# Kernel optimization log

Measured on AMD Instinct MI355X. Metric: run time of the kernel, lower is better.

The kernel has to match this reference:

```python
import jax, jax.numpy as jnp
import numpy as np

B, S, HID = 1, 2048, 2048
HQ, HKV, D = 16, 4, 128
BS = 64            # seerattn gate block size
GH = 128           # gate hidden size
INTER = 5632
THR = 0.004        # seerattn_threshold on softmaxed block gate scores
EPS = 1e-6
NEG = -1e30


def _rms(x, w):
    xf = x.astype(jnp.float32)
    var = jnp.mean(xf * xf, axis=-1, keepdims=True)
    return (w * (xf * jax.lax.rsqrt(var + EPS))).astype(x.dtype)


def _rotate_half(x):
    x1, x2 = jnp.split(x, 2, axis=-1)
    return jnp.concatenate([-x2, x1], axis=-1)


def setup_inputs() -> dict:
    key = jax.random.key(0)
    ks = jax.random.split(key, 16)
    s = 0.02
    pos = jnp.arange(S, dtype=jnp.float32)
    inv_freq = 1.0 / (1e6 ** (jnp.arange(0, D, 2, dtype=jnp.float32) / D))
    freqs = pos[:, None] * inv_freq[None, :]
    emb = jnp.concatenate([freqs, freqs], axis=-1)  # [S, D]
    return {
        'hidden_states': jax.random.normal(ks[0], (B, S, HID), jnp.float32),
        'cos': jnp.cos(emb),
        'sin': jnp.sin(emb),
        'ln1_w': jnp.ones((HID,), jnp.float32),
        'ln2_w': jnp.ones((HID,), jnp.float32),
        'Wq': jax.random.normal(ks[1], (HID, HQ * D), jnp.float32) * s,
        'bq': jnp.zeros((HQ * D,), jnp.float32),
        'Wk': jax.random.normal(ks[2], (HID, HKV * D), jnp.float32) * s,
        'bk': jnp.zeros((HKV * D,), jnp.float32),
        'Wv': jax.random.normal(ks[3], (HID, HKV * D), jnp.float32) * s,
        'bv': jnp.zeros((HKV * D,), jnp.float32),
        'Wo': jax.random.normal(ks[4], (HQ * D, HID), jnp.float32) * s,
        'gWq': jax.random.normal(ks[5], (D, GH), jnp.float32) * s,
        'gWk': jax.random.normal(ks[6], (D, GH), jnp.float32) * s,
        'Wgate': jax.random.normal(ks[7], (HID, INTER), jnp.float32) * s,
        'Wup': jax.random.normal(ks[8], (HID, INTER), jnp.float32) * s,
        'Wdown': jax.random.normal(ks[9], (INTER, HID), jnp.float32) * s,
    }


def reference(hidden_states, cos, sin, ln1_w, ln2_w, Wq, bq, Wk, bk, Wv, bv, Wo,
              gWq, gWk, Wgate, Wup, Wdown):
    B_, S_, _ = hidden_states.shape
    QB = S_ // BS
    grp = HQ // HKV

    h = _rms(hidden_states, ln1_w)
    q = (h @ Wq + bq).reshape(B_, S_, HQ, D)
    k = (h @ Wk + bk).reshape(B_, S_, HKV, D)
    v = (h @ Wv + bv).reshape(B_, S_, HKV, D)

    # ---- learned block gate (pre-RoPE q/k), threshold sparsity method ----
    qg = jnp.einsum('bshd,dg->bshg', q, gWq)
    qg = qg.reshape(B_, QB, BS, HQ, GH).mean(axis=2)            # [B, QB, HQ, GH]
    kp = k.reshape(B_, QB, BS, HKV, D).mean(axis=2)             # block-pooled K
    kg = jnp.einsum('bkhd,dg->bkhg', kp, gWk)
    kg = jnp.repeat(kg, grp, axis=2)                            # GQA -> HQ heads
    gscore = jnp.einsum('bqhg,bkhg->bhqk', qg, kg) * (GH ** -0.5)

    bidx = jnp.arange(QB)
    blk_causal = bidx[:, None] >= bidx[None, :]                 # [QB, QB]
    gscore = jnp.where(blk_causal[None, None], gscore, NEG)
    gate = jax.nn.softmax(gscore, axis=-1)                      # [B, HQ, QB, QB]

    diag = bidx[:, None] == bidx[None, :]
    keep = blk_causal[None, None] & ((gate >= THR) | diag[None, None])

    # ---- RoPE (unsqueeze_dim=2, layout [B,S,H,D]) ----
    c = cos[None, :, None, :]
    sn = sin[None, :, None, :]
    q = q * c + _rotate_half(q) * sn
    k = k * c + _rotate_half(k) * sn

    k = jnp.repeat(k, grp, axis=2)
    v = jnp.repeat(v, grp, axis=2)

    # ---- block-sparse masked attention (reference: dense w/ block mask) ----
    scores = jnp.einsum('bqhd,bkhd->bhqk', q, k) * (D ** -0.5)
    tok_keep = jnp.repeat(jnp.repeat(keep, BS, axis=2), BS, axis=3)
    tidx = jnp.arange(S_)
    tok_causal = tidx[:, None] >= tidx[None, :]
    mask = tok_keep & tok_causal[None, None]
    scores = jnp.where(mask, scores, NEG)
    p = jax.nn.softmax(scores, axis=-1)
    o = jnp.einsum('bhqk,bkhd->bqhd', p, v).reshape(B_, S_, HQ * D)
    attn_out = o @ Wo

    h2 = hidden_states + attn_out
    h3 = _rms(h2, ln2_w)
    mlp = (jax.nn.silu(h3 @ Wgate) * (h3 @ Wup)) @ Wdown
    return h2 + mlp
```

## Files before the change

kernel.cpp:

```cpp
#include <hip/hip_runtime.h>
#include <stdint.h>
#include <stddef.h>

#define S_LEN 2048
#define HIDN  2048
#define HQ    16
#define HKV   4
#define HDIM  128
#define NQKV  3072
#define QBLK  32
#define GHW   128
#define INTER 5632
#define NEGF  (-1e30f)
#define THRG  0.004f

typedef short bf16x8 __attribute__((ext_vector_type(8)));
typedef float f32x4  __attribute__((ext_vector_type(4)));

__device__ __forceinline__ short f2bf(float f) {
  union { float f; unsigned u; } v; v.f = f;
  unsigned r = (v.u + 0x7FFFu + ((v.u >> 16) & 1u)) >> 16;
  return (short)r;
}
__device__ __forceinline__ float bf2f(short s) {
  union { float f; unsigned u; } v; v.u = ((unsigned)(unsigned short)s) << 16;
  return v.f;
}
__device__ __forceinline__ void gload16(const void* g, void* l) {
  __builtin_amdgcn_global_load_lds(
      (const __attribute__((address_space(1))) void*)g,
      (__attribute__((address_space(3))) void*)l, 16, 0, 0);
}
__device__ __forceinline__ unsigned pack_bf2(float hi, float lo) {
  return __builtin_amdgcn_perm(__float_as_uint(hi), __float_as_uint(lo), 0x07060302u);
}

__global__ __launch_bounds__(256) void k_transpose_cast(
    const float* __restrict__ src, short* __restrict__ dst, int R, int C) {
  __shared__ float t[32][33];
  const int tx = threadIdx.x, ty = threadIdx.y;
  const int x = blockIdx.x * 32 + tx;
  const int y0 = blockIdx.y * 32;
#pragma unroll
  for (int i = 0; i < 4; i++) {
    int yy = ty + i * 8;
    t[yy][tx] = src[(long)(y0 + yy) * C + x];
  }
  __syncthreads();
  const int xo = blockIdx.y * 32 + tx;
  const int yo0 = blockIdx.x * 32;
#pragma unroll
  for (int i = 0; i < 4; i++) {
    int yy = ty + i * 8;
    dst[(long)(yo0 + yy) * R + xo] = f2bf(t[tx][yy]);
  }
}

__global__ __launch_bounds__(256) void k_transpose_cast_ilv(
    const float* __restrict__ src, short* __restrict__ dst, int R, int C, int phase) {
  __shared__ float t[32][33];
  const int tx = threadIdx.x, ty = threadIdx.y;
  const int x = blockIdx.x * 32 + tx;
  const int y0 = blockIdx.y * 32;
#pragma unroll
  for (int i = 0; i < 4; i++) {
    int yy = ty + i * 8;
    t[yy][tx] = src[(long)(y0 + yy) * C + x];
  }
  __syncthreads();
  const int xo = blockIdx.y * 32 + tx;
  const int yo0 = blockIdx.x * 32;
#pragma unroll
  for (int i = 0; i < 4; i++) {
    int j = yo0 + ty + i * 8;
    long orow = (long)(j >> 4) * 32 + phase * 16 + (j & 15);
    dst[orow * R + xo] = f2bf(t[tx][ty + i * 8]);
  }
}

__global__ void k_bias_concat(const float* __restrict__ bq, const float* __restrict__ bk,
                              const float* __restrict__ bv, float* __restrict__ out) {
  int i = blockIdx.x * 256 + threadIdx.x;
  if (i < 2048) out[i] = bq[i];
  else if (i < 2560) out[i] = bk[i - 2048];
  else out[i] = bv[i - 2560];
}

__global__ __launch_bounds__(256) void k_rms(const float* __restrict__ x,
                                             const float* __restrict__ w,
                                             short* __restrict__ out) {
  const int row = blockIdx.x;
  const float* xr = x + (long)row * HIDN;
  float v[8];
  float ss = 0.f;
#pragma unroll
  for (int i = 0; i < 8; i++) {
    v[i] = xr[threadIdx.x + i * 256];
    ss += v[i] * v[i];
  }
#pragma unroll
  for (int off = 32; off > 0; off >>= 1) ss += __shfl_down(ss, off, 64);
  __shared__ float red[4];
  const int wave = threadIdx.x >> 6, lane = threadIdx.x & 63;
  if (lane == 0) red[wave] = ss;
  __syncthreads();
  float tot = red[0] + red[1] + red[2] + red[3];
  float rs = rsqrtf(tot / (float)HIDN + 1e-6f);
#pragma unroll
  for (int i = 0; i < 8; i++) {
    int c = threadIdx.x + i * 256;
    out[(long)row * HIDN + c] = f2bf(v[i] * rs * w[c]);
  }
}

__global__ __launch_bounds__(256) void k_rms_fin(const float* __restrict__ p0,
                                                 const float* __restrict__ hid,
                                                 const float* __restrict__ w,
                                                 float* __restrict__ h2,
                                                 short* __restrict__ out) {
  const int row = blockIdx.x;
  const long base = (long)row * HIDN;
  float v[8];
  float ss = 0.f;
#pragma unroll
  for (int i = 0; i < 8; i++) {
    int c = threadIdx.x + i * 256;
    float t = p0[base + c] + h2[base + c] + hid[base + c];
    h2[base + c] = t;
    v[i] = t;
    ss += t * t;
  }
#pragma unroll
  for (int off = 32; off > 0; off >>= 1) ss += __shfl_down(ss, off, 64);
  __shared__ float red[4];
  const int wave = threadIdx.x >> 6, lane = threadIdx.x & 63;
  if (lane == 0) red[wave] = ss;
  __syncthreads();
  float tot = red[0] + red[1] + red[2] + red[3];
  float rs = rsqrtf(tot / (float)HIDN + 1e-6f);
#pragma unroll
  for (int i = 0; i < 8; i++) {
    int c = threadIdx.x + i * 256;
    out[base + c] = f2bf(v[i] * rs * w[c]);
  }
}

template <int MODE, int BN>
__global__ __launch_bounds__(256) void k_gemm(
    const short* __restrict__ A, const short* __restrict__ Bt,
    float* __restrict__ Cf, float* __restrict__ Cf2,
    short* __restrict__ Cb,
    const float* __restrict__ bias, const float* __restrict__ add,
    int M, int N, int K, int ksl) {
  constexpr int NT = BN / 32;
  constexpr int BIW = BN / 32;
  constexpr int BPP = BN / 16;
  __shared__ short As[2][128][32];
  __shared__ short Bs[2][BN][32];
  const int tid = threadIdx.x;
  const int wave = tid >> 6, lane = tid & 63, quad = lane >> 4, l15 = lane & 15;
  const long m0 = (long)blockIdx.y * 128, n0 = (long)blockIdx.x * BN;
  const int wr = (wave >> 1) * 64, wc = (wave & 1) * (BN / 2);
  const int i2 = lane >> 2, i3 = lane & 3;
  f32x4 acc[4][NT] = {};
  const short* Ainst[4];
  short* Alds[4];
#pragma unroll
  for (int j = 0; j < 4; j++) {
    const int g = wave * 4 + j, h = g >> 3, rb = (g & 7) * 16;
    Ainst[j] = A + (m0 + rb + i2) * K + h * 32 + i3 * 8;
    Alds[j] = &As[h][rb][0];
  }
  const short* Binst[BIW];
  short* Blds[BIW];
#pragma unroll
  for (int j = 0; j < BIW; j++) {
    const int g = wave * BIW + j, h = g / BPP, rb = (g % BPP) * 16;
    Binst[j] = Bt + (n0 + rb + i2) * K + h * 32 + i3 * 8;
    Blds[j] = &Bs[h][rb][0];
  }
  const int kbeg = (MODE == 4) ? blockIdx.z * ksl : 0;
  const int kend = kbeg + ((MODE == 4) ? ksl : K);
  for (int k0 = kbeg; k0 < kend; k0 += 64) {
    __syncthreads();
#pragma unroll
    for (int j = 0; j < 4; j++) gload16(Ainst[j] + k0, Alds[j]);
#pragma unroll
    for (int j = 0; j < BIW; j++) gload16(Binst[j] + k0, Blds[j]);
    __syncthreads();
#pragma unroll
    for (int s = 0; s < 2; s++) {
      bf16x8 af[4], bb[NT];
#pragma unroll
      for (int mi = 0; mi < 4; mi++)
        af[mi] = *(const bf16x8*)&As[s][wr + mi * 16 + l15][quad * 8];
#pragma unroll
      for (int ni = 0; ni < NT; ni++)
        bb[ni] = *(const bf16x8*)&Bs[s][wc + ni * 16 + l15][quad * 8];
#pragma unroll
      for (int mi = 0; mi < 4; mi++)
#pragma unroll
        for (int ni = 0; ni < NT; ni++)
          acc[mi][ni] = __builtin_amdgcn_mfma_f32_16x16x32_bf16(af[mi], bb[ni], acc[mi][ni], 0, 0, 0);
    }
  }
  const bool hb = (MODE == 0) && (bias != nullptr);
  const bool ha = (MODE == 0) && (add != nullptr);
  float* dstp = (MODE == 4) ? ((blockIdx.z == 0) ? Cf : Cf2) : Cf;
#pragma unroll
  for (int mi = 0; mi < 4; mi++) {
    if (MODE == 5) {
#pragma unroll
      for (int ni2 = 0; ni2 < NT / 2; ni2++) {
        long mbase = m0 + wr + mi * 16 + quad * 4;
        long col = (n0 + wc) / 2 + ni2 * 16 + l15;
#pragma unroll
        for (int r = 0; r < 4; r++) {
          float g = acc[mi][2 * ni2][r];
          float u = acc[mi][2 * ni2 + 1][r];
          float sg = g / (1.f + __expf(-g));
          Cb[(mbase + r) * INTER + col] = f2bf(sg * u);
        }
      }
    } else {
#pragma unroll
      for (int ni = 0; ni < NT; ni++) {
        long mbase = m0 + wr + mi * 16 + quad * 4;
        long n = n0 + wc + ni * 16 + l15;
#pragma unroll
        for (int r = 0; r < 4; r++) {
          float v = acc[mi][ni][r];
          if (MODE == 0) {
            long idx = (mbase + r) * N + n;
            if (hb) v += bias[n];
            if (ha) v += add[idx];
            Cf[idx] = v;
          } else {
            dstp[(mbase + r) * N + n] = v;
          }
        }
      }
    }
  }
}

__global__ __launch_bounds__(256) void k_finish(const float* __restrict__ p0,
                                                const float* __restrict__ h2,
                                                float* __restrict__ out) {
  const long n = (long)S_LEN * HIDN;
  for (long i = ((long)blockIdx.x * 256 + threadIdx.x) * 4; i < n;
       i += (long)gridDim.x * 256 * 4) {
    float4 a = *(const float4*)(out + i);
    float4 b = *(const float4*)(p0 + i);
    float4 c = *(const float4*)(h2 + i);
    a.x += b.x + c.x;
    a.y += b.y + c.y;
    a.z += b.z + c.z;
    a.w += b.w + c.w;
    *(float4*)(out + i) = a;
  }
}

__global__ __launch_bounds__(256) void k_blockmean(const float* __restrict__ qkv,
                                                   float* __restrict__ qm,
                                                   float* __restrict__ km) {
  int id = blockIdx.x * 256 + threadIdx.x;
  int qb = id / 2560, c = id % 2560;
  const float* base = qkv + (long)qb * 64 * NQKV + c;
  float acc = 0.f;
  for (int s = 0; s < 64; s++) acc += base[(long)s * NQKV];
  acc *= (1.f / 64.f);
  if (c < 2048) qm[(long)qb * 2048 + c] = acc;
  else km[(long)qb * 512 + (c - 2048)] = acc;
}

__global__ __launch_bounds__(128) void k_gateproj(const float* __restrict__ qm,
                                                  const float* __restrict__ km,
                                                  const float* __restrict__ gWq,
                                                  const float* __restrict__ gWk,
                                                  float* __restrict__ qg,
                                                  float* __restrict__ kg) {
  __shared__ float xm[128];
  const int b = blockIdx.x;
  const float* src; const float* W; float* dst;
  if (b < 512) { src = qm + (long)b * 128; W = gWq; dst = qg + (long)b * 128; }
  else { int r = b - 512; src = km + (long)r * 128; W = gWk; dst = kg + (long)r * 128; }
  xm[threadIdx.x] = src[threadIdx.x];
  __syncthreads();
  float acc = 0.f;
  for (int d = 0; d < 128; d++) acc += xm[d] * W[d * GHW + threadIdx.x];
  dst[threadIdx.x] = acc;
}

__global__ __launch_bounds__(64) void k_gatemask(const float* __restrict__ qg,
                                                 const float* __restrict__ kg,
                                                 unsigned char* __restrict__ mask) {
  const int qb = blockIdx.x, h = blockIdx.y;
  __shared__ float qv[128];
  const int t = threadIdx.x;
  qv[t] = qg[((long)qb * 16 + h) * 128 + t];
  qv[t + 64] = qg[((long)qb * 16 + h) * 128 + t + 64];
  __syncthreads();
  const int kb = t;
  float s = NEGF;
  if (kb < 32 && kb <= qb) {
    const float* kr = kg + ((long)kb * 4 + (h >> 2)) * 128;
    float acc = 0.f;
    for (int d = 0; d < 128; d++) acc += qv[d] * kr[d];
    s = acc * 0.08838834764831845f;
  }
  float m = s;
#pragma unroll
  for (int off = 32; off > 0; off >>= 1) m = fmaxf(m, __shfl_xor(m, off, 64));
  float e = (kb < 32 && kb <= qb) ? __expf(s - m) : 0.f;
  float sum = e;
#pragma unroll
  for (int off = 32; off > 0; off >>= 1) sum += __shfl_xor(sum, off, 64);
  if (kb < 32) {
    float gate = e / sum;
    bool keep = (kb <= qb) && (gate >= THRG || kb == qb);
    mask[((long)h * 32 + qb) * 32 + kb] = keep ? 1 : 0;
  }
}

__global__ __launch_bounds__(256) void k_rope(const float* __restrict__ qkv,
                                              const float* __restrict__ cosb,
                                              const float* __restrict__ sinb,
                                              short* __restrict__ q_bf,
                                              short* __restrict__ k_bf) {
  long id = (long)blockIdx.x * 256 + threadIdx.x;
  int d = (int)(id & 63);
  long rest = id >> 6;
  int head = (int)(rest % 20);
  int s = (int)(rest / 20);
  const float c = cosb[(long)s * HDIM + d];
  const float sn = sinb[(long)s * HDIM + d];
  if (head < HQ) {
    const float* src = qkv + (long)s * NQKV + head * HDIM;
    float x1 = src[d], x2 = src[d + 64];
    short* dst = q_bf + ((long)head * S_LEN + s) * HDIM;
    dst[d] = f2bf(x1 * c - x2 * sn);
    dst[d + 64] = f2bf(x2 * c + x1 * sn);
  } else {
    int hk = head - HQ;
    const float* src = qkv + (long)s * NQKV + 2048 + hk * HDIM;
    float x1 = src[d], x2 = src[d + 64];
    short* dst = k_bf + ((long)hk * S_LEN + s) * HDIM;
    dst[d] = f2bf(x1 * c - x2 * sn);
    dst[d + 64] = f2bf(x2 * c + x1 * sn);
  }
}

__global__ __launch_bounds__(256) void k_vcast_t(const float* __restrict__ qkv,
                                                 short* __restrict__ v_t) {
  __shared__ float t[32][33];
  const int hk = blockIdx.z;
  const int tx = threadIdx.x, ty = threadIdx.y;
  const int d0 = blockIdx.x * 32;
  const int s0 = blockIdx.y * 32;
  const float* src = qkv + 2560 + (long)hk * HDIM;
#pragma unroll
  for (int i = 0; i < 4; i++) {
    int s = ty + i * 8;
    t[s][tx] = src[(long)(s0 + s) * NQKV + d0 + tx];
  }
  __syncthreads();
  short* dst = v_t + (long)hk * HDIM * S_LEN;
#pragma unroll
  for (int i = 0; i < 4; i++) {
    int d = ty + i * 8;
    dst[(long)(d0 + d) * S_LEN + s0 + tx] = f2bf(t[tx][d]);
  }
}

__global__ __launch_bounds__(256) void k_attn(const short* __restrict__ q_bf,
                                              const short* __restrict__ k_bf,
                                              const short* __restrict__ v_t,
                                              const unsigned char* __restrict__ mask,
                                              short* __restrict__ o_bf) {
  const int qb = blockIdx.x, h = blockIdx.y;
  const int tid = threadIdx.x, wave = tid >> 6, lane = tid & 63;
  const int quad = lane >> 4, l15 = lane & 15;
  __shared__ short Ks[4 * 64 * 32];
  __shared__ short Vs[2 * 128 * 32];
  __shared__ short Ps[4][16 * 72];
  short* Pw = Ps[wave];
  const int hk = h >> 2;
  const unsigned char* mptr = mask + ((long)h * 32 + qb) * 32;
  const float SCL = 0.08838834764831845f * 1.4426950408889634f;
  const int qrow_g = qb * 64 + wave * 16 + l15;

  bf16x8 bq[4];
  {
    const short* qrp = q_bf + ((long)h * S_LEN + qrow_g) * HDIM + quad * 8;
#pragma unroll
    for (int kd = 0; kd < 4; kd++) bq[kd] = *(const bf16x8*)(qrp + kd * 32);
  }

  const short* kh = k_bf + (long)hk * S_LEN * HDIM;
  const short* vh = v_t + (long)hk * HDIM * S_LEN;

  const int i2 = lane >> 2, i3 = lane & 3;
  int koff[4], voff[4];
  const int vp = wave >> 1, vhh = wave & 1;
#pragma unroll
  for (int inst = 0; inst < 4; inst++) {
    koff[inst] = (inst * 16 + i2) * HDIM + wave * 32 + i3 * 8;
    voff[inst] = (vhh * 64 + inst * 16 + i2) * S_LEN + vp * 32 + i3 * 8;
  }

  f32x4 accO[8] = {};
  float mrow = -3.0e38f, lrow = 0.f;

  for (int kb = 0; kb <= qb; kb++) {
    if (!mptr[kb]) continue;
    __syncthreads();
    {
      const int kg = kb * 64 * HDIM;
      const int vg = kb * 64;
#pragma unroll
      for (int inst = 0; inst < 4; inst++) {
        gload16(kh + kg + koff[inst], &Ks[wave * 2048 + inst * 512]);
        gload16(vh + vg + voff[inst], &Vs[vp * 4096 + (vhh * 64 + inst * 16) * 32]);
      }
    }
    __syncthreads();

    f32x4 sv[4];
#pragma unroll
    for (int nt = 0; nt < 4; nt++) {
      f32x4 t = {};
#pragma unroll
      for (int kd = 0; kd < 4; kd++) {
        bf16x8 ka = *(const bf16x8*)&Ks[kd * 2048 + (nt * 16 + l15) * 32 + quad * 8];
        t = __builtin_amdgcn_mfma_f32_16x16x32_bf16(ka, bq[kd], t, 0, 0, 0);
      }
      sv[nt] = t;
    }
    float lmx = -__builtin_inff();
    if (kb < qb) {
#pragma unroll
      for (int nt = 0; nt < 4; nt++)
#pragma unroll
        for (int r = 0; r < 4; r++) {
          sv[nt][r] *= SCL;
          lmx = fmaxf(lmx, sv[nt][r]);
        }
    } else {
#pragma unroll
      for (int nt = 0; nt < 4; nt++)
#pragma unroll
        for (int r = 0; r < 4; r++) {
          const int kcol = kb * 64 + nt * 16 + quad * 4 + r;
          sv[nt][r] = (kcol <= qrow_g) ? sv[nt][r] * SCL : -__builtin_inff();
          lmx = fmaxf(lmx, sv[nt][r]);
        }
    }
    lmx = fmaxf(lmx, __shfl_xor(lmx, 16, 64));
    lmx = fmaxf(lmx, __shfl_xor(lmx, 32, 64));
    const float mnew = fmaxf(mrow, lmx);
    const float alpha = __builtin_amdgcn_exp2f(mrow - mnew);
    mrow = mnew;
    float psum = 0.f;
#pragma unroll
    for (int nt = 0; nt < 4; nt++) {
#pragma unroll
      for (int r = 0; r < 4; r++) {
        float p = __builtin_amdgcn_exp2f(sv[nt][r] - mnew);
        sv[nt][r] = p;
        psum += p;
      }
      uint2 u;
      u.x = pack_bf2(sv[nt][1], sv[nt][0]);
      u.y = pack_bf2(sv[nt][3], sv[nt][2]);
      *(uint2*)&Pw[l15 * 72 + nt * 16 + quad * 4] = u;
    }
    psum += __shfl_xor(psum, 16, 64);
    psum += __shfl_xor(psum, 32, 64);
    lrow = lrow * alpha + psum;
    float al[4];
#pragma unroll
    for (int r = 0; r < 4; r++) al[r] = __shfl(alpha, quad * 4 + r, 64);
#pragma unroll
    for (int dt = 0; dt < 8; dt++)
#pragma unroll
      for (int r = 0; r < 4; r++) accO[dt][r] *= al[r];
    asm volatile("s_waitcnt lgkmcnt(0)" ::: "memory");
    bf16x8 pf[2];
#pragma unroll
    for (int ksb = 0; ksb < 2; ksb++)
      pf[ksb] = *(const bf16x8*)&Pw[l15 * 72 + ksb * 32 + quad * 8];
#pragma unroll
    for (int dt = 0; dt < 8; dt++) {
#pragma unroll
      for (int ksb = 0; ksb < 2; ksb++) {
        bf16x8 vf = *(const bf16x8*)&Vs[ksb * 4096 + (dt * 16 + l15) * 32 + quad * 8];
        accO[dt] = __builtin_amdgcn_mfma_f32_16x16x32_bf16(pf[ksb], vf, accO[dt], 0, 0, 0);
      }
    }
  }
  const float linv = 1.f / lrow;
  float li[4];
#pragma unroll
  for (int r = 0; r < 4; r++) li[r] = __shfl(linv, quad * 4 + r, 64);
#pragma unroll
  for (int r = 0; r < 4; r++) {
    const long srow = (long)qb * 64 + wave * 16 + quad * 4 + r;
#pragma unroll
    for (int dt = 0; dt < 8; dt++)
      o_bf[srow * HIDN + h * HDIM + dt * 16 + l15] = f2bf(accO[dt][r] * li[r]);
  }
}

static constexpr size_t SZ_WQKVT = (size_t)NQKV * HIDN * 2;
static constexpr size_t SZ_WOT = (size_t)HIDN * HIDN * 2;
static constexpr size_t SZ_WBIG = (size_t)INTER * HIDN * 2;
static constexpr size_t OFF_WQKVT = 0;
static constexpr size_t OFF_WOT = OFF_WQKVT + SZ_WQKVT;
static constexpr size_t OFF_WGU = OFF_WOT + SZ_WOT;
static constexpr size_t OFF_WDOWNT = OFF_WGU + 2 * SZ_WBIG;
static constexpr size_t OFF_BIAS = OFF_WDOWNT + SZ_WBIG;
static constexpr size_t OFF_MASK = OFF_BIAS + 3072 * 4 + 4096;
static constexpr size_t OFF_QM = OFF_MASK + 16 * 32 * 32 + 4096;
static constexpr size_t OFF_KM = OFF_QM + (size_t)32 * 16 * 128 * 4;
static constexpr size_t OFF_QG = OFF_KM + (size_t)32 * 4 * 128 * 4;
static constexpr size_t OFF_KG = OFF_QG + (size_t)32 * 16 * 128 * 4;
static constexpr size_t OFF_H2 = OFF_KG + (size_t)32 * 4 * 128 * 4;
static constexpr size_t OFF_H3 = OFF_H2 + (size_t)S_LEN * HIDN * 4;
static constexpr size_t OFF_REGA = OFF_H3 + (size_t)S_LEN * HIDN * 2;
static constexpr size_t RA_HBF = 0;
static constexpr size_t RA_QBF = RA_HBF + (size_t)S_LEN * HIDN * 2;
static constexpr size_t RA_KBF = RA_QBF + (size_t)HQ * S_LEN * HDIM * 2;
static constexpr size_t RA_VT = RA_KBF + (size_t)HKV * S_LEN * HDIM * 2;
static constexpr size_t RA_OBF = RA_VT + (size_t)HKV * HDIM * S_LEN * 2;
static constexpr size_t SZ_REGA = RA_OBF + (size_t)S_LEN * HIDN * 2;
static constexpr size_t OFF_REGB = OFF_REGA + SZ_REGA;
static constexpr size_t SZ_REGB = (size_t)S_LEN * NQKV * 4;
static constexpr size_t TOTAL_WS = OFF_REGB + SZ_REGB;

extern "C" void kernel_launch(void* const* d_in, const int* in_sizes, int n_in,
                              void* d_out, int out_size, void* d_ws, size_t ws_size,
                              hipStream_t stream) {
  const float* hidden = (const float*)d_in[0];
  const float* cosb = (const float*)d_in[1];
  const float* sinb = (const float*)d_in[2];
  const float* ln1 = (const float*)d_in[3];
  const float* ln2 = (const float*)d_in[4];
  const float* Wq = (const float*)d_in[5];
  const float* bq = (const float*)d_in[6];
  const float* Wk = (const float*)d_in[7];
  const float* bk = (const float*)d_in[8];
  const float* Wv = (const float*)d_in[9];
  const float* bv = (const float*)d_in[10];
  const float* Wo = (const float*)d_in[11];
  const float* gWq = (const float*)d_in[12];
  const float* gWk = (const float*)d_in[13];
  const float* Wgate = (const float*)d_in[14];
  const float* Wup = (const float*)d_in[15];
  const float* Wdown = (const float*)d_in[16];

  if (ws_size < TOTAL_WS) return;

  char* ws = (char*)d_ws;
  short* WqkvT = (short*)(ws + OFF_WQKVT);
  short* WoT = (short*)(ws + OFF_WOT);
  short* Wgu = (short*)(ws + OFF_WGU);
  short* WdownT = (short*)(ws + OFF_WDOWNT);
  float* biasqkv = (float*)(ws + OFF_BIAS);
  unsigned char* maskb = (unsigned char*)(ws + OFF_MASK);
  float* qm = (float*)(ws + OFF_QM);
  float* km = (float*)(ws + OFF_KM);
  float* qg = (float*)(ws + OFF_QG);
  float* kg = (float*)(ws + OFF_KG);
  float* h2 = (float*)(ws + OFF_H2);
  short* h3_bf = (short*)(ws + OFF_H3);
  short* h_bf = (short*)(ws + OFF_REGA + RA_HBF);
  short* q_bf = (short*)(ws + OFF_REGA + RA_QBF);
  short* k_bf = (short*)(ws + OFF_REGA + RA_KBF);
  short* v_t = (short*)(ws + OFF_REGA + RA_VT);
  short* o_bf = (short*)(ws + OFF_REGA + RA_OBF);
  float* p0b = (float*)(ws + OFF_REGA);
  float* qkv_f = (float*)(ws + OFF_REGB);
  float* p0a = (float*)(ws + OFF_REGB);
  short* act_bf = (short*)(ws + OFF_REGB);
  float* outp = (float*)d_out;

  dim3 tb(32, 8);
  k_transpose_cast<<<dim3(64, 64), tb, 0, stream>>>(Wq, WqkvT, HIDN, 2048);
  k_transpose_cast<<<dim3(16, 64), tb, 0, stream>>>(Wk, WqkvT + (size_t)2048 * HIDN, HIDN, 512);
  k_transpose_cast<<<dim3(16, 64), tb, 0, stream>>>(Wv, WqkvT + (size_t)2560 * HIDN, HIDN, 512);
  k_transpose_cast<<<dim3(64, 64), tb, 0, stream>>>(Wo, WoT, HIDN, HIDN);
  k_transpose_cast_ilv<<<dim3(176, 64), tb, 0, stream>>>(Wgate, Wgu, HIDN, INTER, 0);
  k_transpose_cast_ilv<<<dim3(176, 64), tb, 0, stream>>>(Wup, Wgu, HIDN, INTER, 1);
  k_transpose_cast<<<dim3(64, 176), tb, 0, stream>>>(Wdown, WdownT, INTER, HIDN);
  k_bias_concat<<<12, 256, 0, stream>>>(bq, bk, bv, biasqkv);

  k_rms<<<S_LEN, 256, 0, stream>>>(hidden, ln1, h_bf);
  k_gemm<0, 64><<<dim3(NQKV / 64, S_LEN / 128), 256, 0, stream>>>(
      h_bf, WqkvT, qkv_f, nullptr, nullptr, biasqkv, nullptr, S_LEN, NQKV, HIDN, HIDN);
  k_blockmean<<<320, 256, 0, stream>>>(qkv_f, qm, km);
  k_gateproj<<<640, 128, 0, stream>>>(qm, km, gWq, gWk, qg, kg);
  k_gatemask<<<dim3(32, 16), 64, 0, stream>>>(qg, kg, maskb);
  k_rope<<<10240, 256, 0, stream>>>(qkv_f, cosb, sinb, q_bf, k_bf);
  k_vcast_t<<<dim3(4, 64, 4), tb, 0, stream>>>(qkv_f, v_t);
  k_attn<<<dim3(32, 16), 256, 0, stream>>>(q_bf, k_bf, v_t, maskb, o_bf);
  k_gemm<4, 64><<<dim3(HIDN / 64, S_LEN / 128, 2), 256, 0, stream>>>(
      o_bf, WoT, p0a, h2, nullptr, nullptr, nullptr, S_LEN, HIDN, HIDN, HIDN / 2);
  k_rms_fin<<<S_LEN, 256, 0, stream>>>(p0a, hidden, ln2, h2, h3_bf);
  k_gemm<5, 128><<<dim3(2 * INTER / 128, S_LEN / 128), 256, 0, stream>>>(
      h3_bf, Wgu, nullptr, nullptr, act_bf, nullptr, nullptr, S_LEN, 2 * INTER, HIDN, HIDN);
  k_gemm<4, 64><<<dim3(HIDN / 64, S_LEN / 128, 2), 256, 0, stream>>>(
      act_bf, WdownT, p0b, outp, nullptr, nullptr, nullptr, S_LEN, HIDN, INTER, INTER / 2);
  k_finish<<<2048, 256, 0, stream>>>(p0b, h2, outp);
  (void)in_sizes; (void)n_in; (void)out_size;
}
```

Before: 620.6 us.

## Add dedicated 256x128 tile, 512-thread gate/up GEMM with swizzled LDS and BK=64

Replaces the generic MODE 5 gate/up GEMM with a specialized 8-wave kernel using 256x128 output tiles, BK=64 double-buffered direct-to-LDS loads with XOR swizzle, and explicit waitcnt/barrier scheduling plus setprio around MFMAs. The fused SiLU*up epilogue is kept. The aim is more data reuse per tile, fewer LDS bank conflicts and better overlap of loads with MFMA in the largest GEMM. Occupancy drops because of the larger LDS footprint per block. The generic kernel loses its bf16 output parameter.

Result: no change. 631.5 us (+1.8%).

```diff
diff --git a/kernel.cpp b/kernel.cpp
--- a/kernel.cpp
+++ b/kernel.cpp
@@ -149,7 +149,6 @@
 __global__ __launch_bounds__(256) void k_gemm(
     const short* __restrict__ A, const short* __restrict__ Bt,
     float* __restrict__ Cf, float* __restrict__ Cf2,
-    short* __restrict__ Cb,
     const float* __restrict__ bias, const float* __restrict__ add,
     int M, int N, int K, int ksl) {
   constexpr int NT = BN / 32;
@@ -209,36 +208,106 @@
   float* dstp = (MODE == 4) ? ((blockIdx.z == 0) ? Cf : Cf2) : Cf;
 #pragma unroll
   for (int mi = 0; mi < 4; mi++) {
-    if (MODE == 5) {
-#pragma unroll
-      for (int ni2 = 0; ni2 < NT / 2; ni2++) {
-        long mbase = m0 + wr + mi * 16 + quad * 4;
-        long col = (n0 + wc) / 2 + ni2 * 16 + l15;
-#pragma unroll
-        for (int r = 0; r < 4; r++) {
-          float g = acc[mi][2 * ni2][r];
-          float u = acc[mi][2 * ni2 + 1][r];
-          float sg = g / (1.f + __expf(-g));
-          Cb[(mbase + r) * INTER + col] = f2bf(sg * u);
+#pragma unroll
+    for (int ni = 0; ni < NT; ni++) {
+      long mbase = m0 + wr + mi * 16 + quad * 4;
+      long n = n0 + wc + ni * 16 + l15;
+#pragma unroll
+      for (int r = 0; r < 4; r++) {
+        float v = acc[mi][ni][r];
+        if (MODE == 0) {
+          long idx = (mbase + r) * N + n;
+          if (hb) v += bias[n];
+          if (ha) v += add[idx];
+          Cf[idx] = v;
+        } else {
+          dstp[(mbase + r) * N + n] = v;
         }
       }
+    }
+  }
+}
+
+__global__ __launch_bounds__(512) void k_gemm_gu8(
+    const short* __restrict__ A, const short* __restrict__ Bt,
+    short* __restrict__ Cb, int M, int N, int K) {
+  __shared__ short Asl[2][256][64];
+  __shared__ short Bsl[2][128][64];
+  const int tid = threadIdx.x;
+  const int wave = tid >> 6, lane = tid & 63, quad = lane >> 4, l15 = lane & 15;
+  const int wr = (wave & 3) * 64, wc = (wave >> 2) * 64;
+  const long m0 = (long)blockIdx.y * 256, n0 = (long)blockIdx.x * 128;
+  const int rsub = lane >> 3;
+  const int ksw = ((lane & 7) ^ rsub) << 3;
+  const short* aA[4];
+  const short* aB[2];
+#pragma unroll
+  for (int j = 0; j < 4; j++)
+    aA[j] = A + (m0 + (wave * 4 + j) * 8 + rsub) * K + ksw;
+#pragma unroll
+  for (int j = 0; j < 2; j++)
+    aB[j] = Bt + (n0 + (wave * 2 + j) * 8 + rsub) * K + ksw;
+  f32x4 acc[4][4] = {};
+  const int NTI = K >> 6;
+#pragma unroll
+  for (int j = 0; j < 4; j++) gload16(aA[j], &Asl[0][(wave * 4 + j) * 8][0]);
+#pragma unroll
+  for (int j = 0; j < 2; j++) gload16(aB[j], &Bsl[0][(wave * 2 + j) * 8][0]);
+#pragma unroll
+  for (int j = 0; j < 4; j++) gload16(aA[j] + 64, &Asl[1][(wave * 4 + j) * 8][0]);
+#pragma unroll
+  for (int j = 0; j < 2; j++) gload16(aB[j] + 64, &Bsl[1][(wave * 2 + j) * 8][0]);
+  for (int t = 0; t < NTI; ++t) {
+    const int cur = t & 1;
+    if (t + 2 <= NTI) {
+      asm volatile("s_waitcnt vmcnt(6)" ::: "memory");
     } else {
-#pragma unroll
-      for (int ni = 0; ni < NT; ni++) {
-        long mbase = m0 + wr + mi * 16 + quad * 4;
-        long n = n0 + wc + ni * 16 + l15;
-#pragma unroll
-        for (int r = 0; r < 4; r++) {
-          float v = acc[mi][ni][r];
-          if (MODE == 0) {
-            long idx = (mbase + r) * N + n;
-            if (hb) v += bias[n];
-            if (ha) v += add[idx];
-            Cf[idx] = v;
-          } else {
-            dstp[(mbase + r) * N + n] = v;
-          }
-        }
+      asm volatile("s_waitcnt vmcnt(0)" ::: "memory");
+    }
+    __builtin_amdgcn_sched_barrier(0);
+    asm volatile("s_barrier" ::: "memory");
+#pragma unroll
+    for (int kh = 0; kh < 2; kh++) {
+      bf16x8 af[4], bf[4];
+#pragma unroll
+      for (int mi = 0; mi < 4; mi++)
+        af[mi] = *(const bf16x8*)&Asl[cur][wr + mi * 16 + l15]
+                                         [(kh * 32 + quad * 8) ^ ((l15 & 7) << 3)];
+#pragma unroll
+      for (int ni = 0; ni < 4; ni++)
+        bf[ni] = *(const bf16x8*)&Bsl[cur][wc + ni * 16 + l15]
+                                         [(kh * 32 + quad * 8) ^ ((l15 & 7) << 3)];
+      __builtin_amdgcn_s_setprio(1);
+#pragma unroll
+      for (int mi = 0; mi < 4; mi++)
+#pragma unroll
+        for (int ni = 0; ni < 4; ni++)
+          acc[mi][ni] = __builtin_amdgcn_mfma_f32_16x16x32_bf16(af[mi], bf[ni], acc[mi][ni], 0, 0, 0);
+      __builtin_amdgcn_s_setprio(0);
+    }
+    asm volatile("s_waitcnt lgkmcnt(0)" ::: "memory");
+    __builtin_amdgcn_sched_barrier(0);
+    asm volatile("s_barrier" ::: "memory");
+    if (t + 2 < NTI) {
+      const int ko = (t + 2) * 64;
+#pragma unroll
+      for (int j = 0; j < 4; j++) gload16(aA[j] + ko, &Asl[cur][(wave * 4 + j) * 8][0]);
+#pragma unroll
+      for (int j = 0; j < 2; j++) gload16(aB[j] + ko, &Bsl[cur][(wave * 2 + j) * 8][0]);
+    }
+  }
+#pragma unroll
+  for (int mi = 0; mi < 4; mi++) {
+#pragma unroll
+    for (int ni2 = 0; ni2 < 2; ni2++) {
+      long mbase = m0 + wr + mi * 16 + quad * 4;
+      long col = (n0 + wc) / 2 + ni2 * 16 + l15;
+#pragma unroll
+      for (int r = 0; r < 4; r++) {
+        float g = acc[mi][2 * ni2][r];
+        float u = acc[mi][2 * ni2 + 1][r];
+        float sg = g / (1.f + __expf(-g));
+        Cb[(mbase + r) * (N / 2) + col] = f2bf(sg * u);
       }
     }
   }
@@ -597,7 +666,7 @@
 
   k_rms<<<S_LEN, 256, 0, stream>>>(hidden, ln1, h_bf);
   k_gemm<0, 64><<<dim3(NQKV / 64, S_LEN / 128), 256, 0, stream>>>(
-      h_bf, WqkvT, qkv_f, nullptr, nullptr, biasqkv, nullptr, S_LEN, NQKV, HIDN, HIDN);
+      h_bf, WqkvT, qkv_f, nullptr, biasqkv, nullptr, S_LEN, NQKV, HIDN, HIDN);
   k_blockmean<<<320, 256, 0, stream>>>(qkv_f, qm, km);
   k_gateproj<<<640, 128, 0, stream>>>(qm, km, gWq, gWk, qg, kg);
   k_gatemask<<<dim3(32, 16), 64, 0, stream>>>(qg, kg, maskb);
@@ -605,12 +674,12 @@
   k_vcast_t<<<dim3(4, 64, 4), tb, 0, stream>>>(qkv_f, v_t);
   k_attn<<<dim3(32, 16), 256, 0, stream>>>(q_bf, k_bf, v_t, maskb, o_bf);
   k_gemm<4, 64><<<dim3(HIDN / 64, S_LEN / 128, 2), 256, 0, stream>>>(
-      o_bf, WoT, p0a, h2, nullptr, nullptr, nullptr, S_LEN, HIDN, HIDN, HIDN / 2);
+      o_bf, WoT, p0a, h2, nullptr, nullptr, S_LEN, HIDN, HIDN, HIDN / 2);
   k_rms_fin<<<S_LEN, 256, 0, stream>>>(p0a, hidden, ln2, h2, h3_bf);
-  k_gemm<5, 128><<<dim3(2 * INTER / 128, S_LEN / 128), 256, 0, stream>>>(
-      h3_bf, Wgu, nullptr, nullptr, act_bf, nullptr, nullptr, S_LEN, 2 * INTER, HIDN, HIDN);
+  k_gemm_gu8<<<dim3(2 * INTER / 128, S_LEN / 256), 512, 0, stream>>>(
+      h3_bf, Wgu, act_bf, S_LEN, 2 * INTER, HIDN);
   k_gemm<4, 64><<<dim3(HIDN / 64, S_LEN / 128, 2), 256, 0, stream>>>(
-      act_bf, WdownT, p0b, outp, nullptr, nullptr, nullptr, S_LEN, HIDN, INTER, INTER / 2);
+      act_bf, WdownT, p0b, outp, nullptr, nullptr, S_LEN, HIDN, INTER, INTER / 2);
   k_finish<<<2048, 256, 0, stream>>>(p0b, h2, outp);
   (void)in_sizes; (void)n_in; (void)out_size;
 }
```
